# Performance work log

Hardware: AMD Instinct MI355X
Metric: run time of the kernel (lower is better)

Reference implementation:

```python
import jax, jax.numpy as jnp
import numpy as np

B, N, C = 2, 65536, 256
H, D, S = 8, 64, 64  # heads, dim_head, slice_num
INNER = H * D


def setup_inputs() -> dict:
    key = jax.random.key(0)
    ks = jax.random.split(key, 8)
    scale_in = 1.0 / np.sqrt(C)
    scale_d = 1.0 / np.sqrt(D)
    return {
        "x": jax.random.normal(ks[0], (B, N, C), dtype=jnp.float32),
        "W_x": jax.random.uniform(ks[1], (C, INNER), jnp.float32, -scale_in, scale_in),
        "b_x": jax.random.uniform(ks[2], (INNER,), jnp.float32, -scale_in, scale_in),
        "W_fx": jax.random.uniform(ks[3], (C, INNER), jnp.float32, -scale_in, scale_in),
        "b_fx": jax.random.uniform(ks[4], (INNER,), jnp.float32, -scale_in, scale_in),
        "W_slice": jax.random.uniform(ks[5], (D, S), jnp.float32, -scale_d, scale_d),
        "b_slice": jax.random.uniform(ks[6], (S,), jnp.float32, -scale_d, scale_d),
        "temperature": jnp.full((1, H, 1, 1), 0.5, dtype=jnp.float32),
    }


def _split_heads(t):
    # (B, N, H*D) -> (B, H, N, D)
    return t.reshape(B, N, H, D).transpose(0, 2, 1, 3)


def reference(x, W_x, b_x, W_fx, b_fx, W_slice, b_slice, temperature):
    projected_x = _split_heads(x @ W_x + b_x)          # (B,H,N,D)
    fx = _split_heads(x @ W_fx + b_fx)                 # (B,H,N,D)
    slice_proj = projected_x @ W_slice + b_slice       # (B,H,N,S)
    temp = jnp.clip(temperature, 0.5, 5.0)
    slice_weights = jax.nn.softmax(slice_proj / temp, axis=-1)  # (B,H,N,S)
    slice_norm = slice_weights.sum(axis=2)             # (B,H,S)
    normed = slice_weights / (slice_norm[:, :, None, :] + 0.01)
    # weighted token aggregation: (B,H,S,D)
    slice_tokens = jnp.einsum("bhns,bhnd->bhsd", normed, fx)
    return slice_tokens
```

## Files before the change

kernel.cpp:

```cpp
#include <hip/hip_runtime.h>

typedef _Float16 f16;
typedef __attribute__((ext_vector_type(8))) _Float16 f16x8;
typedef __attribute__((ext_vector_type(4))) _Float16 f16x4;
typedef __attribute__((ext_vector_type(4))) float    f32x4;

#define MFMA(a,b,c) __builtin_amdgcn_mfma_f32_16x16x32_f16(a,b,c,0,0,0)

constexpr int Bc = 2, Nc = 65536, Cc = 256, Hc = 8;
constexpr int CHUNK = 512;
constexpr int LDX = 72;
constexpr int LDT = 136;


__device__ __forceinline__ f32x4 splat4(float v) { f32x4 r; r.x=v; r.y=v; r.z=v; r.w=v; return r; }
__device__ __forceinline__ f16x8 pack8(float4 a, float4 b) {
  f16x8 r = { (f16)a.x,(f16)a.y,(f16)a.z,(f16)a.w,(f16)b.x,(f16)b.y,(f16)b.z,(f16)b.w };
  return r;
}

__global__ void prep_a(const float* __restrict__ Wx, const float* __restrict__ Wfx,
                       const float* __restrict__ Wsl, const float* __restrict__ bx,
                       const float* __restrict__ bsl, f16* __restrict__ WC,
                       float* __restrict__ bsp) {
  __shared__ float tile[64][72];
  const int b = blockIdx.x, t = threadIdx.x;
  if (b < 32) {
    const int k0 = (b & 3) * 64, c0 = (b >> 2) * 64;
    const int r = t >> 4, c4 = (t & 15) * 4;
    #pragma unroll
    for (int i = 0; i < 4; ++i) {
      float4 v = *(const float4*)&Wfx[(size_t)(k0 + r + i*16)*512 + c0 + c4];
      tile[r + i*16][c4] = v.x; tile[r + i*16][c4+1] = v.y;
      tile[r + i*16][c4+2] = v.z; tile[r + i*16][c4+3] = v.w;
    }
    __syncthreads();
    const int cl = t >> 2, kq = t & 3;
    const int col = c0 + cl, h = col >> 6, n = col & 63;
    f16 tmp[16];
    #pragma unroll
    for (int j = 0; j < 16; ++j) tmp[j] = (f16)tile[kq*16 + j][cl];
    f16* dst = WC + (size_t)(h*128 + n)*256 + k0 + kq*16;
    *(f16x8*)dst       = *(f16x8*)&tmp[0];
    *(f16x8*)(dst + 8) = *(f16x8*)&tmp[8];
  } else if (b < 96) {
    const int bb = b - 32;
    const int h = bb >> 3, k0 = (bb & 7) * 32;
    const int k = t & 31, sq = t >> 5;
    float accs[8];
    #pragma unroll
    for (int j = 0; j < 8; ++j) accs[j] = 0.f;
    for (int d = 0; d < 64; ++d) {
      float a = Wx[(size_t)(k0 + k)*512 + h*64 + d];
      #pragma unroll
      for (int j = 0; j < 8; ++j) accs[j] += a * Wsl[d*64 + sq*8 + j];
    }
    #pragma unroll
    for (int j = 0; j < 8; ++j)
      WC[(size_t)(h*128 + 64 + sq*8 + j)*256 + k0 + k] = (f16)accs[j];
  } else {
    for (int u = t; u < 512; u += 256) {
      int h = u >> 6, s = u & 63;
      float a = bsl[s];
      for (int d = 0; d < 64; ++d) a += bx[h*64 + d] * Wsl[d*64 + s];
      bsp[h*64 + s] = a;
    }
  }
}

__global__ __launch_bounds__(256, 2)
void fused_main(const float* __restrict__ x,   const float* __restrict__ bfx,
                const float* __restrict__ bsp, const float* __restrict__ temp,
                const f16* __restrict__ WC,    float* __restrict__ Tg,
                float* __restrict__ normg) {
  __shared__ alignas(16) char smem[2 * 128 * LDX * 2];
  f16* sm_x   = (f16*)smem;
  f16* sm_w   = (f16*)(smem + 128*LDX*2);
  f16* sm_fxT = sm_x;
  f16* sm_wT  = sm_w;

  const int j    = blockIdx.x;
  const int xcd  = j & 7, slot = j >> 3;
  const int chunk = xcd * 32 + (slot >> 3);
  const int h     = slot & 7;

  const int tid = threadIdx.x;
  const int wv = tid >> 6, lane = tid & 63, quad = lane >> 4, ln = lane & 15;
  const int wm = wv >> 1, wn = wv & 1;
  const long tokBase = (long)chunk * CHUNK;
  const int b  = (int)(tokBase >> 16);
  const int bh = b * Hc + h;

  const float tc = fminf(fmaxf(temp[h], 0.5f), 5.0f);
  const float k2 = 1.44269504f / tc;

  float bv[4];
  {
    const float* bb = (wn == 0) ? (bfx + h*64) : (bsp + h*64);
    #pragma unroll
    for (int nt = 0; nt < 4; ++nt) bv[nt] = bb[nt*16 + ln];
  }

  f32x4 Tacc[2][2];
  #pragma unroll
  for (int i = 0; i < 2; ++i) { Tacc[i][0] = splat4(0.f); Tacc[i][1] = splat4(0.f); }
  float nacc[4] = {0.f, 0.f, 0.f, 0.f};
  const int ci = wv >> 1, cj = wv & 1;

  const f16* WCh = WC + (size_t)h * 128 * 256;

  const int r0 = tid >> 2, seg = tid & 3;
  const int wrow = tid >> 1, whalf = tid & 1;

  float4 xr[8]; f16x8 wr[4];
  auto loadx = [&](int m0, int kb) {
    const float* p = x + (tokBase + (long)m0*128 + r0)*Cc + kb*64 + seg*16;
    xr[0] = *(const float4*)p;        xr[1] = *(const float4*)(p + 4);
    xr[2] = *(const float4*)(p + 8);  xr[3] = *(const float4*)(p + 12);
    p += 64 * Cc;
    xr[4] = *(const float4*)p;        xr[5] = *(const float4*)(p + 4);
    xr[6] = *(const float4*)(p + 8);  xr[7] = *(const float4*)(p + 12);
  };
  auto loadw = [&](int kb) {
    const f16* p = WCh + wrow*256 + kb*64 + whalf*32;
    wr[0] = *(const f16x8*)p;         wr[1] = *(const f16x8*)(p + 8);
    wr[2] = *(const f16x8*)(p + 16);  wr[3] = *(const f16x8*)(p + 24);
  };

  loadx(0, 0); loadw(0);

  for (int m0 = 0; m0 < 4; ++m0) {
    f32x4 acc[4][4];
    #pragma unroll
    for (int mt = 0; mt < 4; ++mt)
      #pragma unroll
      for (int nt = 0; nt < 4; ++nt) acc[mt][nt] = splat4(bv[nt]);

    for (int kb = 0; kb < 4; ++kb) {
      __syncthreads();
      *(f16x8*)&sm_x[r0*LDX + seg*16]          = pack8(xr[0], xr[1]);
      *(f16x8*)&sm_x[r0*LDX + seg*16 + 8]      = pack8(xr[2], xr[3]);
      *(f16x8*)&sm_x[(r0+64)*LDX + seg*16]     = pack8(xr[4], xr[5]);
      *(f16x8*)&sm_x[(r0+64)*LDX + seg*16 + 8] = pack8(xr[6], xr[7]);
      *(f16x8*)&sm_w[wrow*LDX + whalf*32]      = wr[0];
      *(f16x8*)&sm_w[wrow*LDX + whalf*32 +  8] = wr[1];
      *(f16x8*)&sm_w[wrow*LDX + whalf*32 + 16] = wr[2];
      *(f16x8*)&sm_w[wrow*LDX + whalf*32 + 24] = wr[3];
      { int nkb = kb + 1, nm0 = m0;
        if (nkb == 4) { nkb = 0; ++nm0; }
        if (nm0 < 4) { loadx(nm0, nkb); loadw(nkb); } }
      __syncthreads();
      #pragma unroll
      for (int ks = 0; ks < 2; ++ks) {
        f16x8 af[4], bf[4];
        #pragma unroll
        for (int mt = 0; mt < 4; ++mt)
          af[mt] = *(const f16x8*)&sm_x[(wm*64 + mt*16 + ln)*LDX + ks*32 + quad*8];
        #pragma unroll
        for (int nt = 0; nt < 4; ++nt)
          bf[nt] = *(const f16x8*)&sm_w[(wn*64 + nt*16 + ln)*LDX + ks*32 + quad*8];
        #pragma unroll
        for (int mt = 0; mt < 4; ++mt)
          #pragma unroll
          for (int nt = 0; nt < 4; ++nt)
            acc[mt][nt] = MFMA(af[mt], bf[nt], acc[mt][nt]);
      }
    }
    __syncthreads();

    if (wn == 0) {
      #pragma unroll
      for (int mt = 0; mt < 4; ++mt)
        #pragma unroll
        for (int nt = 0; nt < 4; ++nt) {
          f16x4 v = { (f16)acc[mt][nt][0], (f16)acc[mt][nt][1],
                      (f16)acc[mt][nt][2], (f16)acc[mt][nt][3] };
          *(f16x4*)&sm_fxT[(nt*16 + ln)*LDT + wm*64 + mt*16 + quad*4] = v;
        }
    } else {
      #pragma unroll
      for (int mt = 0; mt < 4; ++mt) {
        float e[4][4], wout[4][4];
        #pragma unroll
        for (int nt = 0; nt < 4; ++nt)
          #pragma unroll
          for (int rg = 0; rg < 4; ++rg)
            e[nt][rg] = exp2f(acc[mt][nt][rg] * k2);
        #pragma unroll
        for (int rg = 0; rg < 4; ++rg) {
          float rs = e[0][rg] + e[1][rg] + e[2][rg] + e[3][rg];
          #pragma unroll
          for (int dd = 1; dd < 16; dd <<= 1) rs += __shfl_xor(rs, dd, 64);
          float inv = 1.0f / rs;
          #pragma unroll
          for (int nt = 0; nt < 4; ++nt) {
            wout[nt][rg] = e[nt][rg] * inv;
            nacc[nt] += wout[nt][rg];
          }
        }
        #pragma unroll
        for (int nt = 0; nt < 4; ++nt) {
          f16x4 v = { (f16)wout[nt][0], (f16)wout[nt][1],
                      (f16)wout[nt][2], (f16)wout[nt][3] };
          *(f16x4*)&sm_wT[(nt*16 + ln)*LDT + wm*64 + mt*16 + quad*4] = v;
        }
      }
    }
    __syncthreads();

    #pragma unroll
    for (int ks = 0; ks < 4; ++ks) {
      f16x8 a0 = *(const f16x8*)&sm_wT [(ci*32 +      ln)*LDT + ks*32 + quad*8];
      f16x8 a1 = *(const f16x8*)&sm_wT [(ci*32 + 16 + ln)*LDT + ks*32 + quad*8];
      f16x8 b0 = *(const f16x8*)&sm_fxT[(cj*32 +      ln)*LDT + ks*32 + quad*8];
      f16x8 b1 = *(const f16x8*)&sm_fxT[(cj*32 + 16 + ln)*LDT + ks*32 + quad*8];
      Tacc[0][0] = MFMA(a0, b0, Tacc[0][0]);
      Tacc[0][1] = MFMA(a0, b1, Tacc[0][1]);
      Tacc[1][0] = MFMA(a1, b0, Tacc[1][0]);
      Tacc[1][1] = MFMA(a1, b1, Tacc[1][1]);
    }
  }

  float* Tb = Tg + bh * 4096;
  #pragma unroll
  for (int mt2 = 0; mt2 < 2; ++mt2)
    #pragma unroll
    for (int nt2 = 0; nt2 < 2; ++nt2)
      #pragma unroll
      for (int rg = 0; rg < 4; ++rg) {
        int s = ci*32 + mt2*16 + quad*4 + rg;
        int d = cj*32 + nt2*16 + ln;
        atomicAdd(&Tb[s*64 + d], Tacc[mt2][nt2][rg]);
      }
  if (wn == 1) {
    #pragma unroll
    for (int nt = 0; nt < 4; ++nt) {
      float v = nacc[nt];
      v += __shfl_xor(v, 16, 64);
      v += __shfl_xor(v, 32, 64);
      if (lane < 16) atomicAdd(&normg[bh*64 + nt*16 + ln], v);
    }
  }
}

__global__ void finalize(const float* __restrict__ Tg, const float* __restrict__ normg,
                         float* __restrict__ out) {
  int i = blockIdx.x * 256 + threadIdx.x;
  out[i] = Tg[i] / (normg[i >> 6] + 0.01f);
}

extern "C" void kernel_launch(void* const* d_in, const int* in_sizes, int n_in,
                              void* d_out, int out_size, void* d_ws, size_t ws_size,
                              hipStream_t stream) {
  const float* x    = (const float*)d_in[0];
  const float* Wx   = (const float*)d_in[1];
  const float* bx   = (const float*)d_in[2];
  const float* Wfx  = (const float*)d_in[3];
  const float* bfx  = (const float*)d_in[4];
  const float* Wsl  = (const float*)d_in[5];
  const float* bsl  = (const float*)d_in[6];
  const float* temp = (const float*)d_in[7];
  float* out = (float*)d_out;

  float* Tg    = (float*)d_ws;
  float* normg = Tg + 16 * 4096;
  f16*   WC    = (f16*)((char*)d_ws + 266240);
  float* bsp   = (float*)((char*)d_ws + 790528);

  hipMemsetAsync(d_ws, 0, 266240, stream);
  prep_a    <<<97, 256, 0, stream>>>(Wx, Wfx, Wsl, bx, bsl, WC, bsp);
  fused_main<<<2048, 256, 0, stream>>>(x, bfx, bsp, temp, WC, Tg, normg);
  finalize  <<<256, 256, 0, stream>>>(Tg, normg, out);
}
```

Baseline: 346.4 us.

## Pre-convert x to swizzled fp16 and DMA tiles directly into LDS

Adds a new path, taken when the workspace is large enough, that first converts x to fp16 with an XOR-swizzled layout and relayouts the weights the same way. The main kernel then loads tiles with global_load_lds DMA instead of register-staged fp32 loads. Per-chunk partial results are written to a buffer and summed in finalize, replacing atomics and the memset. This trades an extra full pass over x (read fp32, write fp16) plus a large partial buffer for cheaper main-loop loads and no atomic contention.

```diff
diff --git a/kernel.cpp b/kernel.cpp
--- a/kernel.cpp
+++ b/kernel.cpp
@@ -7,11 +7,7 @@
 
 #define MFMA(a,b,c) __builtin_amdgcn_mfma_f32_16x16x32_f16(a,b,c,0,0,0)
 
-constexpr int Bc = 2, Nc = 65536, Cc = 256, Hc = 8;
-constexpr int CHUNK = 512;
-constexpr int LDX = 72;
-constexpr int LDT = 136;
-
+constexpr int Hc = 8;
 
 __device__ __forceinline__ f32x4 splat4(float v) { f32x4 r; r.x=v; r.y=v; r.z=v; r.w=v; return r; }
 __device__ __forceinline__ f16x8 pack8(float4 a, float4 b) {
@@ -19,15 +15,256 @@
   return r;
 }
 
-__global__ void prep_a(const float* __restrict__ Wx, const float* __restrict__ Wfx,
+typedef __attribute__((address_space(1))) void gvoid;
+typedef __attribute__((address_space(3))) void lvoid;
+__device__ __forceinline__ void dma16(const void* g, void* l) {
+  __builtin_amdgcn_global_load_lds((gvoid*)g, (lvoid*)l, 16, 0, 0);
+}
+
+
+__global__ void prep_all(const float* __restrict__ x,   const float* __restrict__ Wx,
+                         const float* __restrict__ Wfx, const float* __restrict__ Wsl,
+                         const float* __restrict__ bx,  const float* __restrict__ bsl,
+                         f16* __restrict__ xh, f16* __restrict__ WC, float* __restrict__ bsp) {
+  __shared__ float tile[64][72];
+  const int b = blockIdx.x, t = threadIdx.x;
+  if (b < 1024) {
+    #pragma unroll
+    for (int it = 0; it < 16; ++it) {
+      int G = b*4096 + it*256 + t;
+      int tok = G >> 5, pos = G & 31;
+      size_t base = (size_t)tok*256 + (pos >> 3)*64;
+      int p = pos & 7;
+      const float* src = x + base + p*8;
+      float4 v0 = *(const float4*)src;
+      float4 v1 = *(const float4*)(src + 4);
+      *(f16x8*)&xh[base + ((p ^ (tok & 7))*8)] = pack8(v0, v1);
+    }
+  } else if (b < 1056) {
+    const int bb = b - 1024;
+    const int kb = bb & 3, c0 = (bb >> 2)*64, k0 = kb*64;
+    const int r = t >> 4, c4 = (t & 15)*4;
+    #pragma unroll
+    for (int i = 0; i < 4; ++i) {
+      float4 v = *(const float4*)&Wfx[(size_t)(k0 + r + i*16)*512 + c0 + c4];
+      tile[r + i*16][c4] = v.x; tile[r + i*16][c4+1] = v.y;
+      tile[r + i*16][c4+2] = v.z; tile[r + i*16][c4+3] = v.w;
+    }
+    __syncthreads();
+    const int cl = t >> 2, kq = t & 3;
+    const int col = c0 + cl, h = col >> 6, n = col & 63;
+    f16 tmp[16];
+    #pragma unroll
+    for (int jj = 0; jj < 16; ++jj) tmp[jj] = (f16)tile[kq*16 + jj][cl];
+    size_t rowbase = ((size_t)(h*4 + kb)*128 + n)*64;
+    *(f16x8*)&WC[rowbase + ((2*kq    ) ^ (n & 7))*8] = *(f16x8*)&tmp[0];
+    *(f16x8*)&WC[rowbase + ((2*kq + 1) ^ (n & 7))*8] = *(f16x8*)&tmp[8];
+  } else if (b < 1120) {
+    const int bb = b - 1056;
+    const int h = bb >> 3, k0 = (bb & 7)*32;
+    const int k = t & 31, sq = t >> 5;
+    float accs[8];
+    #pragma unroll
+    for (int jj = 0; jj < 8; ++jj) accs[jj] = 0.f;
+    for (int d = 0; d < 64; ++d) {
+      float a = Wx[(size_t)(k0 + k)*512 + h*64 + d];
+      #pragma unroll
+      for (int jj = 0; jj < 8; ++jj) accs[jj] += a * Wsl[d*64 + sq*8 + jj];
+    }
+    const int kb = k0 >> 6, kl = (k0 & 63) + k;
+    const int p = kl >> 3, off = kl & 7;
+    #pragma unroll
+    for (int jj = 0; jj < 8; ++jj) {
+      int n = 64 + sq*8 + jj;
+      WC[((size_t)(h*4 + kb)*128 + n)*64 + (p ^ (n & 7))*8 + off] = (f16)accs[jj];
+    }
+  } else {
+    for (int u = t; u < 512; u += 256) {
+      int h = u >> 6, s = u & 63;
+      float a = bsl[s];
+      for (int d = 0; d < 64; ++d) a += bx[h*64 + d] * Wsl[d*64 + s];
+      bsp[h*64 + s] = a;
+    }
+  }
+}
+
+__global__ __launch_bounds__(256, 2)
+void fused_a(const f16* __restrict__ xh, const float* __restrict__ bfx,
+             const float* __restrict__ bsp, const float* __restrict__ temp,
+             const f16* __restrict__ WC, float* __restrict__ P, float* __restrict__ Pn) {
+  __shared__ alignas(16) f16 sm_x[8192];
+  __shared__ alignas(16) f16 sm_w[8192];
+  f16* fxT = sm_x;
+  f16* wT  = sm_w;
+
+  const int j    = blockIdx.x;
+  const int xcd  = j & 7, slot = j >> 3;
+  const int chunk = xcd*32 + (slot >> 3);
+  const int h     = slot & 7;
+
+  const int tid = threadIdx.x;
+  const int wv = tid >> 6, lane = tid & 63, quad = lane >> 4, ln = lane & 15;
+  const int wm = wv >> 1, wn = wv & 1;
+  const int ci = wv >> 1, cj = wv & 1;
+  const long tokBase = (long)chunk * 512;
+  const int bIdx = (int)(tokBase >> 16);
+  const int bh = bIdx*Hc + h;
+  const int c  = chunk & 127;
+
+  const float tc = fminf(fmaxf(temp[h], 0.5f), 5.0f);
+  const float k2 = 1.44269504f / tc;
+
+  float bv[4];
+  { const float* bb = wn ? (bsp + h*64) : (bfx + h*64);
+    #pragma unroll
+    for (int nt = 0; nt < 4; ++nt) bv[nt] = bb[nt*16 + ln]; }
+
+  f32x4 Tacc[2][2];
+  #pragma unroll
+  for (int i = 0; i < 2; ++i) { Tacc[i][0] = splat4(0.f); Tacc[i][1] = splat4(0.f); }
+  float nacc[4] = {0.f, 0.f, 0.f, 0.f};
+
+  const f16* WCh = WC + (size_t)h * 32768;
+  const int lrow = lane >> 3, lcol = lane & 7;
+  const f16* xlane = xh + (tokBase + lrow)*256 + lcol*8;
+  const f16* wlane = WCh + lane*8;
+
+  for (int m0 = 0; m0 < 4; ++m0) {
+    f32x4 acc[4][4];
+    #pragma unroll
+    for (int mt = 0; mt < 4; ++mt)
+      #pragma unroll
+      for (int nt = 0; nt < 4; ++nt) acc[mt][nt] = splat4(bv[nt]);
+
+    for (int kb = 0; kb < 4; ++kb) {
+      __syncthreads();
+      #pragma unroll
+      for (int i = 0; i < 4; ++i) {
+        int seg = 4*wv + i;
+        dma16(xlane + (size_t)(m0*128 + seg*8)*256 + kb*64, &sm_x[seg*512]);
+        dma16(wlane + (size_t)kb*8192 + seg*512,            &sm_w[seg*512]);
+      }
+      __syncthreads();
+      #pragma unroll
+      for (int ks = 0; ks < 2; ++ks) {
+        const int qo = ((ks*4 + quad) ^ (ln & 7)) * 8;
+        f16x8 af[4], bf[4];
+        #pragma unroll
+        for (int mt = 0; mt < 4; ++mt)
+          af[mt] = *(const f16x8*)&sm_x[(wm*64 + mt*16 + ln)*64 + qo];
+        #pragma unroll
+        for (int nt = 0; nt < 4; ++nt)
+          bf[nt] = *(const f16x8*)&sm_w[(wn*64 + nt*16 + ln)*64 + qo];
+        #pragma unroll
+        for (int mt = 0; mt < 4; ++mt)
+          #pragma unroll
+          for (int nt = 0; nt < 4; ++nt)
+            acc[mt][nt] = MFMA(af[mt], bf[nt], acc[mt][nt]);
+      }
+    }
+    __syncthreads();
+
+    if (wn == 0) {
+      #pragma unroll
+      for (int mt = 0; mt < 4; ++mt) {
+        const int p = wm*8 + mt*2 + (quad >> 1), ho = (quad & 1)*4;
+        #pragma unroll
+        for (int nt = 0; nt < 4; ++nt) {
+          f16x4 v = { (f16)acc[mt][nt][0], (f16)acc[mt][nt][1],
+                      (f16)acc[mt][nt][2], (f16)acc[mt][nt][3] };
+          *(f16x4*)&fxT[(nt*16 + ln)*128 + (p ^ ln)*8 + ho] = v;
+        }
+      }
+    } else {
+      #pragma unroll
+      for (int mt = 0; mt < 4; ++mt) {
+        const int p = wm*8 + mt*2 + (quad >> 1), ho = (quad & 1)*4;
+        float e[4][4], wout[4][4];
+        #pragma unroll
+        for (int nt = 0; nt < 4; ++nt)
+          #pragma unroll
+          for (int rg = 0; rg < 4; ++rg)
+            e[nt][rg] = exp2f(acc[mt][nt][rg] * k2);
+        #pragma unroll
+        for (int rg = 0; rg < 4; ++rg) {
+          float rs = e[0][rg] + e[1][rg] + e[2][rg] + e[3][rg];
+          #pragma unroll
+          for (int dd = 1; dd < 16; dd <<= 1) rs += __shfl_xor(rs, dd, 64);
+          float inv = 1.0f / rs;
+          #pragma unroll
+          for (int nt = 0; nt < 4; ++nt) {
+            wout[nt][rg] = e[nt][rg] * inv;
+            nacc[nt] += wout[nt][rg];
+          }
+        }
+        #pragma unroll
+        for (int nt = 0; nt < 4; ++nt) {
+          f16x4 v = { (f16)wout[nt][0], (f16)wout[nt][1],
+                      (f16)wout[nt][2], (f16)wout[nt][3] };
+          *(f16x4*)&wT[(nt*16 + ln)*128 + (p ^ ln)*8 + ho] = v;
+        }
+      }
+    }
+    __syncthreads();
+
+    #pragma unroll
+    for (int ks = 0; ks < 4; ++ks) {
+      const int q = (ks*4 + quad) ^ ln;
+      f16x8 a0 = *(const f16x8*)&wT [(ci*32      + ln)*128 + q*8];
+      f16x8 a1 = *(const f16x8*)&wT [(ci*32 + 16 + ln)*128 + q*8];
+      f16x8 b0 = *(const f16x8*)&fxT[(cj*32      + ln)*128 + q*8];
+      f16x8 b1 = *(const f16x8*)&fxT[(cj*32 + 16 + ln)*128 + q*8];
+      Tacc[0][0] = MFMA(a0, b0, Tacc[0][0]);
+      Tacc[0][1] = MFMA(a0, b1, Tacc[0][1]);
+      Tacc[1][0] = MFMA(a1, b0, Tacc[1][0]);
+      Tacc[1][1] = MFMA(a1, b1, Tacc[1][1]);
+    }
+  }
+
+  float* Pb = P + (size_t)c*65536 + bh*4096;
+  #pragma unroll
+  for (int mt2 = 0; mt2 < 2; ++mt2)
+    #pragma unroll
+    for (int nt2 = 0; nt2 < 2; ++nt2)
+      #pragma unroll
+      for (int rg = 0; rg < 4; ++rg)
+        Pb[(ci*32 + mt2*16 + quad*4 + rg)*64 + cj*32 + nt2*16 + ln] = Tacc[mt2][nt2][rg];
+  if (wn == 1) {
+    #pragma unroll
+    for (int nt = 0; nt < 4; ++nt) {
+      float v = nacc[nt];
+      v += __shfl_xor(v, 16, 64);
+      v += __shfl_xor(v, 32, 64);
+      if (lane < 16) Pn[((size_t)c*2 + wm)*1024 + bh*64 + nt*16 + ln] = v;
+    }
+  }
+}
+
+__global__ void finalize_a(const float* __restrict__ P, const float* __restrict__ Pn,
+                           float* __restrict__ out) {
+  int i = blockIdx.x*256 + threadIdx.x;
+  float s = 0.f;
+  #pragma unroll 4
+  for (int cc = 0; cc < 128; ++cc) s += P[(size_t)cc*65536 + i];
+  int ns = i >> 6;
+  float nv = 0.f;
+  #pragma unroll 4
+  for (int cc = 0; cc < 256; ++cc) nv += Pn[(size_t)cc*1024 + ns];
+  out[i] = s / (nv + 0.01f);
+}
+
+constexpr int LDX = 72;
+constexpr int LDT = 136;
+
+__global__ void prep_b(const float* __restrict__ Wx, const float* __restrict__ Wfx,
                        const float* __restrict__ Wsl, const float* __restrict__ bx,
                        const float* __restrict__ bsl, f16* __restrict__ WC,
                        float* __restrict__ bsp) {
   __shared__ float tile[64][72];
   const int b = blockIdx.x, t = threadIdx.x;
   if (b < 32) {
-    const int k0 = (b & 3) * 64, c0 = (b >> 2) * 64;
-    const int r = t >> 4, c4 = (t & 15) * 4;
+    const int k0 = (b & 3)*64, c0 = (b >> 2)*64;
+    const int r = t >> 4, c4 = (t & 15)*4;
     #pragma unroll
     for (int i = 0; i < 4; ++i) {
       float4 v = *(const float4*)&Wfx[(size_t)(k0 + r + i*16)*512 + c0 + c4];
@@ -39,25 +276,25 @@
     const int col = c0 + cl, h = col >> 6, n = col & 63;
     f16 tmp[16];
     #pragma unroll
-    for (int j = 0; j < 16; ++j) tmp[j] = (f16)tile[kq*16 + j][cl];
+    for (int jj = 0; jj < 16; ++jj) tmp[jj] = (f16)tile[kq*16 + jj][cl];
     f16* dst = WC + (size_t)(h*128 + n)*256 + k0 + kq*16;
     *(f16x8*)dst       = *(f16x8*)&tmp[0];
     *(f16x8*)(dst + 8) = *(f16x8*)&tmp[8];
   } else if (b < 96) {
     const int bb = b - 32;
-    const int h = bb >> 3, k0 = (bb & 7) * 32;
+    const int h = bb >> 3, k0 = (bb & 7)*32;
     const int k = t & 31, sq = t >> 5;
     float accs[8];
     #pragma unroll
-    for (int j = 0; j < 8; ++j) accs[j] = 0.f;
+    for (int jj = 0; jj < 8; ++jj) accs[jj] = 0.f;
     for (int d = 0; d < 64; ++d) {
       float a = Wx[(size_t)(k0 + k)*512 + h*64 + d];
       #pragma unroll
-      for (int j = 0; j < 8; ++j) accs[j] += a * Wsl[d*64 + sq*8 + j];
-    }
-    #pragma unroll
-    for (int j = 0; j < 8; ++j)
-      WC[(size_t)(h*128 + 64 + sq*8 + j)*256 + k0 + k] = (f16)accs[j];
+      for (int jj = 0; jj < 8; ++jj) accs[jj] += a * Wsl[d*64 + sq*8 + jj];
+    }
+    #pragma unroll
+    for (int jj = 0; jj < 8; ++jj)
+      WC[(size_t)(h*128 + 64 + sq*8 + jj)*256 + k0 + k] = (f16)accs[jj];
   } else {
     for (int u = t; u < 512; u += 256) {
       int h = u >> 6, s = u & 63;
@@ -69,10 +306,10 @@
 }
 
 __global__ __launch_bounds__(256, 2)
-void fused_main(const float* __restrict__ x,   const float* __restrict__ bfx,
-                const float* __restrict__ bsp, const float* __restrict__ temp,
-                const f16* __restrict__ WC,    float* __restrict__ Tg,
-                float* __restrict__ normg) {
+void fused_b(const float* __restrict__ x,   const float* __restrict__ bfx,
+             const float* __restrict__ bsp, const float* __restrict__ temp,
+             const f16* __restrict__ WC,    float* __restrict__ Tg,
+             float* __restrict__ normg) {
   __shared__ alignas(16) char smem[2 * 128 * LDX * 2];
   f16* sm_x   = (f16*)smem;
   f16* sm_w   = (f16*)(smem + 128*LDX*2);
@@ -81,25 +318,23 @@
 
   const int j    = blockIdx.x;
   const int xcd  = j & 7, slot = j >> 3;
-  const int chunk = xcd * 32 + (slot >> 3);
+  const int chunk = xcd*32 + (slot >> 3);
   const int h     = slot & 7;
 
   const int tid = threadIdx.x;
   const int wv = tid >> 6, lane = tid & 63, quad = lane >> 4, ln = lane & 15;
   const int wm = wv >> 1, wn = wv & 1;
-  const long tokBase = (long)chunk * CHUNK;
+  const long tokBase = (long)chunk * 512;
   const int b  = (int)(tokBase >> 16);
-  const int bh = b * Hc + h;
+  const int bh = b*Hc + h;
 
   const float tc = fminf(fmaxf(temp[h], 0.5f), 5.0f);
   const float k2 = 1.44269504f / tc;
 
   float bv[4];
-  {
-    const float* bb = (wn == 0) ? (bfx + h*64) : (bsp + h*64);
-    #pragma unroll
-    for (int nt = 0; nt < 4; ++nt) bv[nt] = bb[nt*16 + ln];
-  }
+  { const float* bb = (wn == 0) ? (bfx + h*64) : (bsp + h*64);
+    #pragma unroll
+    for (int nt = 0; nt < 4; ++nt) bv[nt] = bb[nt*16 + ln]; }
 
   f32x4 Tacc[2][2];
   #pragma unroll
@@ -108,16 +343,15 @@
   const int ci = wv >> 1, cj = wv & 1;
 
   const f16* WCh = WC + (size_t)h * 128 * 256;
-
   const int r0 = tid >> 2, seg = tid & 3;
   const int wrow = tid >> 1, whalf = tid & 1;
 
   float4 xr[8]; f16x8 wr[4];
   auto loadx = [&](int m0, int kb) {
-    const float* p = x + (tokBase + (long)m0*128 + r0)*Cc + kb*64 + seg*16;
+    const float* p = x + (tokBase + (long)m0*128 + r0)*256 + kb*64 + seg*16;
     xr[0] = *(const float4*)p;        xr[1] = *(const float4*)(p + 4);
     xr[2] = *(const float4*)(p + 8);  xr[3] = *(const float4*)(p + 12);
-    p += 64 * Cc;
+    p += 64 * 256;
     xr[4] = *(const float4*)p;        xr[5] = *(const float4*)(p + 4);
     xr[6] = *(const float4*)(p + 8);  xr[7] = *(const float4*)(p + 12);
   };
@@ -210,9 +444,9 @@
 
     #pragma unroll
     for (int ks = 0; ks < 4; ++ks) {
-      f16x8 a0 = *(const f16x8*)&sm_wT [(ci*32 +      ln)*LDT + ks*32 + quad*8];
+      f16x8 a0 = *(const f16x8*)&sm_wT [(ci*32      + ln)*LDT + ks*32 + quad*8];
       f16x8 a1 = *(const f16x8*)&sm_wT [(ci*32 + 16 + ln)*LDT + ks*32 + quad*8];
-      f16x8 b0 = *(const f16x8*)&sm_fxT[(cj*32 +      ln)*LDT + ks*32 + quad*8];
+      f16x8 b0 = *(const f16x8*)&sm_fxT[(cj*32      + ln)*LDT + ks*32 + quad*8];
       f16x8 b1 = *(const f16x8*)&sm_fxT[(cj*32 + 16 + ln)*LDT + ks*32 + quad*8];
       Tacc[0][0] = MFMA(a0, b0, Tacc[0][0]);
       Tacc[0][1] = MFMA(a0, b1, Tacc[0][1]);
@@ -243,9 +477,9 @@
   }
 }
 
-__global__ void finalize(const float* __restrict__ Tg, const float* __restrict__ normg,
-                         float* __restrict__ out) {
-  int i = blockIdx.x * 256 + threadIdx.x;
+__global__ void finalize_b(const float* __restrict__ Tg, const float* __restrict__ normg,
+                           float* __restrict__ out) {
+  int i = blockIdx.x*256 + threadIdx.x;
   out[i] = Tg[i] / (normg[i >> 6] + 0.01f);
 }
 
@@ -262,13 +496,24 @@
   const float* temp = (const float*)d_in[7];
   float* out = (float*)d_out;
 
-  float* Tg    = (float*)d_ws;
-  float* normg = Tg + 16 * 4096;
-  f16*   WC    = (f16*)((char*)d_ws + 266240);
-  float* bsp   = (float*)((char*)d_ws + 790528);
-
-  hipMemsetAsync(d_ws, 0, 266240, stream);
-  prep_a    <<<97, 256, 0, stream>>>(Wx, Wfx, Wsl, bx, bsl, WC, bsp);
-  fused_main<<<2048, 256, 0, stream>>>(x, bfx, bsp, temp, WC, Tg, normg);
-  finalize  <<<256, 256, 0, stream>>>(Tg, normg, out);
-}
+  const size_t NEED = 102238208;
+  if (ws_size >= NEED) {
+    f16*   xh  = (f16*)d_ws;
+    f16*   WC  = (f16*)((char*)d_ws + 67108864);
+    float* bsp = (float*)((char*)d_ws + 67633152);
+    float* P   = (float*)((char*)d_ws + 67635200);
+    float* Pn  = (float*)((char*)d_ws + 101189632);
+    prep_all  <<<1121, 256, 0, stream>>>(x, Wx, Wfx, Wsl, bx, bsl, xh, WC, bsp);
+    fused_a   <<<2048, 256, 0, stream>>>(xh, bfx, bsp, temp, WC, P, Pn);
+    finalize_a<<<256, 256, 0, stream>>>(P, Pn, out);
+  } else {
+    float* Tg    = (float*)d_ws;
+    float* normg = Tg + 16*4096;
+    f16*   WC    = (f16*)((char*)d_ws + 266240);
+    float* bsp   = (float*)((char*)d_ws + 790528);
+    hipMemsetAsync(d_ws, 0, 266240, stream);
+    prep_b    <<<97, 256, 0, stream>>>(Wx, Wfx, Wsl, bx, bsl, WC, bsp);
+    fused_b   <<<2048, 256, 0, stream>>>(x, bfx, bsp, temp, WC, Tg, normg);
+    finalize_b<<<256, 256, 0, stream>>>(Tg, normg, out);
+  }
+}
```

Result: slower. 375.6 us (+8.4%).
